# Kernel optimization log

Hardware: AMD Instinct MI355X
Metric: run time of the kernel (lower is better)

The kernel has to match this reference:

```python
import jax, jax.numpy as jnp
import numpy as np

D_MODEL = 1024
NUM_HEADS = 16
D_K = D_MODEL // NUM_HEADS


def setup_inputs() -> dict:
    key = jax.random.key(0)
    ks = jax.random.split(key, 9)
    s = 1.0 / np.sqrt(D_MODEL)
    x = jax.random.normal(ks[0], (4, 2048, D_MODEL), dtype=jnp.float32)
    Wq = jax.random.uniform(ks[1], (D_MODEL, D_MODEL), jnp.float32, -s, s)
    bq = jax.random.uniform(ks[2], (D_MODEL,), jnp.float32, -s, s)
    Wk = jax.random.uniform(ks[3], (D_MODEL, D_MODEL), jnp.float32, -s, s)
    bk = jax.random.uniform(ks[4], (D_MODEL,), jnp.float32, -s, s)
    Wv = jax.random.uniform(ks[5], (D_MODEL, D_MODEL), jnp.float32, -s, s)
    bv = jax.random.uniform(ks[6], (D_MODEL,), jnp.float32, -s, s)
    Wo = jax.random.uniform(ks[7], (D_MODEL, D_MODEL), jnp.float32, -s, s)
    bo = jax.random.uniform(ks[8], (D_MODEL,), jnp.float32, -s, s)
    return {"x": x, "Wq": Wq, "bq": bq, "Wk": Wk, "bk": bk,
            "Wv": Wv, "bv": bv, "Wo": Wo, "bo": bo}


def reference(x, Wq, bq, Wk, bk, Wv, bv, Wo, bo):
    B, S, _ = x.shape
    # Linear projections (torch Linear: x @ W.T + b)
    q = x @ Wq.T + bq
    k = x @ Wk.T + bk
    v = x @ Wv.T + bv
    # [B, H, S, d_k]
    q = q.reshape(B, S, NUM_HEADS, D_K).transpose(0, 2, 1, 3)
    k = k.reshape(B, S, NUM_HEADS, D_K).transpose(0, 2, 1, 3)
    v = v.reshape(B, S, NUM_HEADS, D_K).transpose(0, 2, 1, 3)
    score = jnp.einsum('bhqd,bhkd->bhqk', q, k) / jnp.sqrt(jnp.float32(D_K))
    causal = jnp.tril(jnp.ones((S, S), dtype=bool))  # True = keep
    score = jnp.where(causal[None, None], score, -jnp.inf)
    attn = jax.nn.softmax(score, axis=-1)
    out = jnp.einsum('bhqk,bhkd->bhqd', attn, v)
    out = out.transpose(0, 2, 1, 3).reshape(B, S, D_MODEL)
    return out @ Wo.T + bo
```

## Files before the change

### kernel.cpp

```cpp
#include <hip/hip_runtime.h>
#include <hip/hip_bf16.h>
#include <stdint.h>

#define D_MODEL 1024
#define SEQ     2048
#define BATCH   4
#define NHEAD   16
#define DKH     64
#define MTOT    (BATCH * SEQ)

typedef __bf16 bf16x8 __attribute__((ext_vector_type(8)));
typedef __bf16 bf16x4 __attribute__((ext_vector_type(4)));
typedef float  floatx4 __attribute__((ext_vector_type(4)));
typedef short  s16x4  __attribute__((ext_vector_type(4)));

#define GLOAD_LDS16(gp, lp)                                            \
    __builtin_amdgcn_global_load_lds(                                  \
        (const __attribute__((address_space(1))) unsigned int*)(gp),   \
        (__attribute__((address_space(3))) unsigned int*)(lp), 16, 0, 0)

#define MFMA16(a, b, c) __builtin_amdgcn_mfma_f32_16x16x32_bf16(a, b, c, 0, 0, 0)

#if __has_builtin(__builtin_amdgcn_exp2f)
#define EXP2(x) __builtin_amdgcn_exp2f(x)
#else
#define EXP2(x) exp2f(x)
#endif

static __device__ __forceinline__ floatx4 pv_mfma(s16x4 a, s16x4 b, floatx4 c)
{
#if __has_builtin(__builtin_amdgcn_mfma_f32_16x16x16bf16_1k)
    return __builtin_amdgcn_mfma_f32_16x16x16bf16_1k(a, b, c, 0, 0, 0);
#else
    asm("v_mfma_f32_16x16x16_bf16 %0, %1, %2, %0" : "+v"(c) : "v"(a), "v"(b));
    return c;
#endif
}

__global__ __launch_bounds__(256)
void cvt_x_kernel(const float* __restrict__ src, __bf16* __restrict__ dst)
{
    const int i = (blockIdx.x * 256 + threadIdx.x) * 4;
    floatx4 v = *(const floatx4*)(src + i);
    bf16x4 o;
    o[0] = (__bf16)v[0]; o[1] = (__bf16)v[1]; o[2] = (__bf16)v[2]; o[3] = (__bf16)v[3];
    *(bf16x4*)(dst + i) = o;
}

__global__ __launch_bounds__(256)
void cvt_w3_kernel(const float* __restrict__ Wq, const float* __restrict__ Wk,
                   const float* __restrict__ Wv, __bf16* __restrict__ Wcat)
{
    const int z = blockIdx.y;
    const float* src = (z == 0) ? Wq : ((z == 1) ? Wk : Wv);
    const int i = (blockIdx.x * 256 + threadIdx.x) * 4;
    floatx4 v = *(const floatx4*)(src + i);
    bf16x4 o;
    o[0] = (__bf16)v[0]; o[1] = (__bf16)v[1]; o[2] = (__bf16)v[2]; o[3] = (__bf16)v[3];
    *(bf16x4*)(Wcat + (size_t)z * (D_MODEL * D_MODEL) + i) = o;
}

__global__ __launch_bounds__(256)
void qkv_gemm_kernel(const __bf16* __restrict__ xb, const __bf16* __restrict__ Wcat,
                     const float* __restrict__ bq, const float* __restrict__ bk,
                     const float* __restrict__ bv,
                     __bf16* __restrict__ Q, __bf16* __restrict__ K,
                     __bf16* __restrict__ Vt)
{
    __shared__ __align__(16) char smem_raw[128 * 136 * 2];
    __bf16* As = (__bf16*)smem_raw;
    __bf16* Bs = (__bf16*)(smem_raw + 8192);
    __bf16* Cs = (__bf16*)smem_raw;

    const int t    = threadIdx.x;
    const int w    = t >> 6, l = t & 63, quad = l >> 4, r16 = l & 15;
    const int wm   = w & 1, wn = w >> 1;
    const int m0   = blockIdx.y * 128;
    const int n0   = blockIdx.x * 128;
    const int z    = n0 >> 10;
    const float* bias = (z == 0) ? bq : ((z == 1) ? bk : bv);
    __bf16* outQK     = (z == 0) ? Q  : K;
    const float scale = (z == 0) ? 0.18033688011112042f : 1.0f;

    floatx4 acc[4][4];
#pragma unroll
    for (int i = 0; i < 4; ++i)
#pragma unroll
        for (int j = 0; j < 4; ++j) acc[i][j] = (floatx4){0.f, 0.f, 0.f, 0.f};

    const int c0 = t, c1 = t + 256;
    const int row0 = c0 >> 2, s0 = ((c0 & 3) ^ (row0 & 3)) * 8;
    const int row1 = c1 >> 2, s1 = ((c1 & 3) ^ (row1 & 3)) * 8;
    const __bf16* Ag0 = xb   + (size_t)(m0 + row0) * 1024 + s0;
    const __bf16* Ag1 = xb   + (size_t)(m0 + row1) * 1024 + s1;
    const __bf16* Bg0 = Wcat + (size_t)(n0 + row0) * 1024 + s0;
    const __bf16* Bg1 = Wcat + (size_t)(n0 + row1) * 1024 + s1;
    unsigned int* lAs = (unsigned int*)As;
    unsigned int* lBs = (unsigned int*)Bs;

    const int fsw = (quad ^ (r16 & 3)) * 8;

    for (int k0 = 0; k0 < 1024; k0 += 32) {
        __syncthreads();
        GLOAD_LDS16(Ag0 + k0, lAs + c0 * 4);
        GLOAD_LDS16(Ag1 + k0, lAs + c1 * 4);
        GLOAD_LDS16(Bg0 + k0, lBs + c0 * 4);
        GLOAD_LDS16(Bg1 + k0, lBs + c1 * 4);
        __syncthreads();

        bf16x8 af[4], bfm[4];
#pragma unroll
        for (int i = 0; i < 4; ++i)
            af[i] = *(const bf16x8*)&As[(wm * 64 + i * 16 + r16) * 32 + fsw];
#pragma unroll
        for (int j = 0; j < 4; ++j)
            bfm[j] = *(const bf16x8*)&Bs[(wn * 64 + j * 16 + r16) * 32 + fsw];
#pragma unroll
        for (int i = 0; i < 4; ++i)
#pragma unroll
            for (int j = 0; j < 4; ++j)
                acc[i][j] = MFMA16(af[i], bfm[j], acc[i][j]);
    }

    __syncthreads();

    if (z == 2) {
#pragma unroll
        for (int i = 0; i < 4; ++i) {
            const int mb = wm * 64 + i * 16 + quad * 4;
#pragma unroll
            for (int j = 0; j < 4; ++j) {
                const int nl = wn * 64 + j * 16 + r16;
                const float bb = bias[(n0 + nl) & 1023];
                bf16x4 p4;
#pragma unroll
                for (int r = 0; r < 4; ++r) p4[r] = (__bf16)(acc[i][j][r] + bb);
                *(bf16x4*)&Cs[nl * 136 + mb] = p4;
            }
        }
    } else {
#pragma unroll
        for (int i = 0; i < 4; ++i) {
            const int mb = wm * 64 + i * 16 + quad * 4;
#pragma unroll
            for (int j = 0; j < 4; ++j) {
                const int nl = wn * 64 + j * 16 + r16;
                const float bb = bias[(n0 + nl) & 1023];
#pragma unroll
                for (int r = 0; r < 4; ++r)
                    Cs[(mb + r) * 136 + nl] =
                        (__bf16)((acc[i][j][r] + bb) * scale);
            }
        }
    }
    __syncthreads();

    const int b  = m0 >> 11;
    if (z == 2) {
#pragma unroll
        for (int k = 0; k < 8; ++k) {
            const int nl = (t >> 4) + k * 16;
            const int ml = (t & 15) * 8;
            bf16x8 row = *(const bf16x8*)&Cs[nl * 136 + ml];
            const int f = (n0 + nl) & 1023, h = f >> 6, d = f & 63;
            const int s = (m0 & 2047) + ml;
            *(bf16x8*)&Vt[((size_t)((b * 16 + h) * 64 + d) << 11) + s] = row;
        }
    } else {
#pragma unroll
        for (int k = 0; k < 8; ++k) {
            const int ml = (t >> 4) + k * 16;
            const int nl = (t & 15) * 8;
            bf16x8 row = *(const bf16x8*)&Cs[ml * 136 + nl];
            const int f = (n0 + nl) & 1023, h = f >> 6, d = f & 63;
            const int s = (m0 & 2047) + ml;
            *(bf16x8*)&outQK[((size_t)(b * 16 + h) << 17) + ((size_t)s << 6) + d]
                = row;
        }
    }
}

__global__ __launch_bounds__(256)
void out_gemm_kernel(const __bf16* __restrict__ A, const __bf16* __restrict__ Wob,
                     const float* __restrict__ bo, float* __restrict__ out)
{
    __shared__ __align__(16) __bf16 As[128 * 64];
    __shared__ __align__(16) __bf16 Bs[128 * 64];

    const int t    = threadIdx.x;
    const int w    = t >> 6, l = t & 63, quad = l >> 4, r16 = l & 15;
    const int wm   = w & 1, wn = w >> 1;
    const int m0   = blockIdx.x * 128;
    const int n0   = blockIdx.y * 128;

    floatx4 acc[4][4];
#pragma unroll
    for (int i = 0; i < 4; ++i)
#pragma unroll
        for (int j = 0; j < 4; ++j) acc[i][j] = (floatx4){0.f, 0.f, 0.f, 0.f};

    unsigned int* lAs = (unsigned int*)As;
    unsigned int* lBs = (unsigned int*)Bs;

    const int r0 = t >> 3;
    const __bf16* Agp[4];
    const __bf16* Bgp[4];
#pragma unroll
    for (int i = 0; i < 4; ++i) {
        const int row = r0 + i * 32;
        const int sch8 = ((t & 7) ^ (row & 7)) * 8;
        Agp[i] = A   + (size_t)(m0 + row) * 1024 + sch8;
        Bgp[i] = Wob + (size_t)(n0 + row) * 1024 + sch8;
    }
    const int fsw0 = ((0 * 4 + quad) ^ (r16 & 7)) * 8;
    const int fsw1 = ((1 * 4 + quad) ^ (r16 & 7)) * 8;

    for (int k0 = 0; k0 < 1024; k0 += 64) {
        __syncthreads();
#pragma unroll
        for (int i = 0; i < 4; ++i) {
            const int c = t + 256 * i;
            GLOAD_LDS16(Agp[i] + k0, lAs + c * 4);
            GLOAD_LDS16(Bgp[i] + k0, lBs + c * 4);
        }
        __syncthreads();

#pragma unroll
        for (int kk = 0; kk < 2; ++kk) {
            const int fsw = (kk == 0) ? fsw0 : fsw1;
            bf16x8 af[4], bfm[4];
#pragma unroll
            for (int i = 0; i < 4; ++i)
                af[i] = *(const bf16x8*)&As[(wm * 64 + i * 16 + r16) * 64 + fsw];
#pragma unroll
            for (int j = 0; j < 4; ++j)
                bfm[j] = *(const bf16x8*)&Bs[(wn * 64 + j * 16 + r16) * 64 + fsw];
#pragma unroll
            for (int i = 0; i < 4; ++i)
#pragma unroll
                for (int j = 0; j < 4; ++j)
                    acc[i][j] = MFMA16(af[i], bfm[j], acc[i][j]);
        }
    }

#pragma unroll
    for (int i = 0; i < 4; ++i) {
        const int mg = m0 + wm * 64 + i * 16 + quad * 4;
#pragma unroll
        for (int j = 0; j < 4; ++j) {
            const int ng = n0 + wn * 64 + j * 16 + r16;
            const float bb = bo[ng];
#pragma unroll
            for (int r = 0; r < 4; ++r)
                out[(size_t)(mg + r) * 1024 + ng] = acc[i][j][r] + bb;
        }
    }
}

__global__ __launch_bounds__(256, 4)
void attn_kernel(const __bf16* __restrict__ Qg, const __bf16* __restrict__ Kg,
                 const __bf16* __restrict__ Vtg, __bf16* __restrict__ O)
{
    __shared__ __align__(16) __bf16 Ks[2][64 * 72];
    __shared__ __align__(16) __bf16 Vs[2][64 * 72];

    const int t    = threadIdx.x;
    const int w    = t >> 6, l = t & 63, quad = l >> 4, r16 = l & 15;
    const int bh   = blockIdx.x;
    const int y    = blockIdx.y;
    const int p    = y >> 1, half = y & 1;
    const int qa   = 15 - p, qb = p;
    const size_t base = (size_t)bh * SEQ * DKH;
    const int d0   = 2 * qa + half;
    const int d1   = 2 * qb + half;
    const int nkt  = d0 + 1;
    const int row0 = qa * 128 + half * 64 + w * 16;
    const int row1 = qb * 128 + half * 64 + w * 16;

    const s16x4 ones16 = {(short)0x3F80, (short)0x3F80,
                          (short)0x3F80, (short)0x3F80};

    bf16x8 qf00, qf01, qf10, qf11;
    qf00 = *(const bf16x8*)&Qg[base + (size_t)(row0 + r16) * 64 + quad * 8];
    qf01 = *(const bf16x8*)&Qg[base + (size_t)(row0 + r16) * 64 + 32 + quad * 8];
    qf10 = *(const bf16x8*)&Qg[base + (size_t)(row1 + r16) * 64 + quad * 8];
    qf11 = *(const bf16x8*)&Qg[base + (size_t)(row1 + r16) * 64 + 32 + quad * 8];

    floatx4 o[2][4];
#pragma unroll
    for (int mi = 0; mi < 2; ++mi)
#pragma unroll
        for (int j = 0; j < 4; ++j) o[mi][j] = (floatx4){0.f, 0.f, 0.f, 0.f};
    floatx4 osum[2];
    osum[0] = (floatx4){0.f, 0.f, 0.f, 0.f};
    osum[1] = (floatx4){0.f, 0.f, 0.f, 0.f};

    const int srow = t >> 3;
    const int sg   = (t & 7) * 8;

    bf16x8 kc0, kc1, vc0, vc1;
    kc0 = *(const bf16x8*)&Kg[base + (size_t)srow * 64 + sg];
    kc1 = *(const bf16x8*)&Kg[base + (size_t)(32 + srow) * 64 + sg];
    vc0 = *(const bf16x8*)&Vtg[base + (size_t)srow * 2048 + sg];
    vc1 = *(const bf16x8*)&Vtg[base + (size_t)(32 + srow) * 2048 + sg];

    for (int kt = 0; kt < nkt; ++kt) {
        __bf16* ks = Ks[kt & 1];
        __bf16* vs = Vs[kt & 1];
        *(bf16x8*)&ks[srow * 72 + sg] = kc0;
        *(bf16x8*)&ks[(32 + srow) * 72 + sg] = kc1;
        *(bf16x8*)&vs[srow * 72 + sg] = vc0;
        *(bf16x8*)&vs[(32 + srow) * 72 + sg] = vc1;
        if (kt + 1 < nkt) {
            const int kr = (kt + 1) * 64;
            kc0 = *(const bf16x8*)&Kg[base + (size_t)(kr + srow) * 64 + sg];
            kc1 = *(const bf16x8*)&Kg[base + (size_t)(kr + 32 + srow) * 64 + sg];
            vc0 = *(const bf16x8*)&Vtg[base + (size_t)srow * 2048 + kr + sg];
            vc1 = *(const bf16x8*)&Vtg[base + (size_t)(32 + srow) * 2048 + kr + sg];
        }
        __syncthreads();

        const bool a1 = (kt <= d1);
        __builtin_amdgcn_s_setprio(1);
        bf16x8 kf0, kf1;
#pragma unroll
        for (int j = 0; j < 4; ++j) {
            kf0 = *(const bf16x8*)&ks[(j * 16 + r16) * 72 + quad * 8];
            kf1 = *(const bf16x8*)&ks[(j * 16 + r16) * 72 + 32 + quad * 8];
            floatx4 z0 = (floatx4){0.f, 0.f, 0.f, 0.f};
            floatx4 z1 = (floatx4){0.f, 0.f, 0.f, 0.f};
            z0 = MFMA16(kf0, qf00, z0);
            z0 = MFMA16(kf1, qf01, z0);
            if (a1) {
                z1 = MFMA16(kf0, qf10, z1);
                z1 = MFMA16(kf1, qf11, z1);
            }
            const int kg = kt * 64 + j * 16 + quad * 4;
            bf16x4 pb0, pb1;
            if (kt < d0) {
#pragma unroll
                for (int r = 0; r < 4; ++r)
                    pb0[r] = (__bf16)EXP2(z0[r]);
            } else {
                const int qg0 = row0 + r16;
#pragma unroll
                for (int r = 0; r < 4; ++r) {
                    float pp = 0.f;
                    if (kg + r <= qg0) pp = EXP2(z0[r]);
                    pb0[r] = (__bf16)pp;
                }
            }
            s16x4 pa0 = __builtin_bit_cast(s16x4, pb0);
            s16x4 pa1;
            if (a1) {
                if (kt < d1) {
#pragma unroll
                    for (int r = 0; r < 4; ++r)
                        pb1[r] = (__bf16)EXP2(z1[r]);
                } else {
                    const int qg1 = row1 + r16;
#pragma unroll
                    for (int r = 0; r < 4; ++r) {
                        float pp = 0.f;
                        if (kg + r <= qg1) pp = EXP2(z1[r]);
                        pb1[r] = (__bf16)pp;
                    }
                }
                pa1 = __builtin_bit_cast(s16x4, pb1);
            }
            osum[0] = pv_mfma(pa0, ones16, osum[0]);
            if (a1) osum[1] = pv_mfma(pa1, ones16, osum[1]);
#pragma unroll
            for (int jd = 0; jd < 4; ++jd) {
                const s16x4 vv =
                    *(const s16x4*)&vs[(jd * 16 + r16) * 72 + j * 16 + quad * 4];
                o[0][jd] = pv_mfma(pa0, vv, o[0][jd]);
                if (a1) o[1][jd] = pv_mfma(pa1, vv, o[1][jd]);
            }
        }
        __builtin_amdgcn_s_setprio(0);
    }

    const int b = bh >> 4, h = bh & 15;
#pragma unroll
    for (int mi = 0; mi < 2; ++mi) {
        const int rowb = (mi == 0) ? row0 : row1;
#pragma unroll
        for (int r = 0; r < 4; ++r) {
            const int qrow = rowb + quad * 4 + r;
            const float inv = 1.f / osum[mi][r];
#pragma unroll
            for (int jd = 0; jd < 4; ++jd) {
                const int d = jd * 16 + r16;
                O[((size_t)(b * SEQ + qrow) * D_MODEL) + h * 64 + d] =
                    (__bf16)(o[mi][jd][r] * inv);
            }
        }
    }
}

extern "C" void kernel_launch(void* const* d_in, const int* in_sizes, int n_in,
                              void* d_out, int out_size, void* d_ws, size_t ws_size,
                              hipStream_t stream)
{
    (void)in_sizes; (void)n_in; (void)out_size; (void)ws_size;
    const float* x  = (const float*)d_in[0];
    const float* Wq = (const float*)d_in[1];
    const float* bq = (const float*)d_in[2];
    const float* Wk = (const float*)d_in[3];
    const float* bk = (const float*)d_in[4];
    const float* Wv = (const float*)d_in[5];
    const float* bv = (const float*)d_in[6];
    const float* Wo = (const float*)d_in[7];
    const float* bo = (const float*)d_in[8];
    float* out = (float*)d_out;

    const size_t n_elem = (size_t)MTOT * D_MODEL;
    const int    w_n    = D_MODEL * D_MODEL;
    __bf16* Qb  = (__bf16*)d_out;
    __bf16* xb  = Qb + n_elem;
    __bf16* Kb   = (__bf16*)d_ws;
    __bf16* Vtb  = Kb + n_elem;
    __bf16* Ab   = Vtb + n_elem;
    __bf16* Wcat = Ab;
    __bf16* Wob  = Kb;

    cvt_x_kernel<<<MTOT * D_MODEL / 1024, 256, 0, stream>>>(x, xb);
    cvt_w3_kernel<<<dim3(w_n / 1024, 3), 256, 0, stream>>>(Wq, Wk, Wv, Wcat);
    qkv_gemm_kernel<<<dim3(24, 64), 256, 0, stream>>>(xb, Wcat, bq, bk, bv,
                                                      Qb, Kb, Vtb);
    attn_kernel<<<dim3(64, 16), 256, 0, stream>>>(Qb, Kb, Vtb, Ab);
    cvt_x_kernel<<<w_n / 1024, 256, 0, stream>>>(Wo, Wob);
    out_gemm_kernel<<<dim3(64, 8), 256, 0, stream>>>(Ab, Wob, bo, out);
}
```

Measured before the change: 246.2 us.

## Enlarge QKV GEMM block tile to 256x128 with 512 threads

The QKV projection GEMM now uses 512-thread blocks computing 256x128 output tiles instead of 256x128-thread 128x128 tiles, halving the grid along M. Each B (weight) tile loaded into LDS is reused by twice as many rows, which cuts global weight traffic per FLOP. The epilogue is split into two passes that reuse the same LDS staging buffer, adding extra barriers. Fewer blocks (768) and higher LDS per block may reduce occupancy and latency hiding.

```diff
diff --git a/kernel.cpp b/kernel.cpp
--- a/kernel.cpp
+++ b/kernel.cpp
@@ -60,22 +60,22 @@
     *(bf16x4*)(Wcat + (size_t)z * (D_MODEL * D_MODEL) + i) = o;
 }
 
-__global__ __launch_bounds__(256)
+__global__ __launch_bounds__(512)
 void qkv_gemm_kernel(const __bf16* __restrict__ xb, const __bf16* __restrict__ Wcat,
                      const float* __restrict__ bq, const float* __restrict__ bk,
                      const float* __restrict__ bv,
                      __bf16* __restrict__ Q, __bf16* __restrict__ K,
                      __bf16* __restrict__ Vt)
 {
-    __shared__ __align__(16) char smem_raw[128 * 136 * 2];
+    __shared__ __align__(16) char smem_raw[34816];
     __bf16* As = (__bf16*)smem_raw;
-    __bf16* Bs = (__bf16*)(smem_raw + 8192);
+    __bf16* Bs = (__bf16*)(smem_raw + 16384);
     __bf16* Cs = (__bf16*)smem_raw;
 
     const int t    = threadIdx.x;
     const int w    = t >> 6, l = t & 63, quad = l >> 4, r16 = l & 15;
-    const int wm   = w & 1, wn = w >> 1;
-    const int m0   = blockIdx.y * 128;
+    const int wm   = w >> 1, wn = w & 1;
+    const int m0   = blockIdx.y * 256;
     const int n0   = blockIdx.x * 128;
     const int z    = n0 >> 10;
     const float* bias = (z == 0) ? bq : ((z == 1) ? bk : bv);
@@ -88,13 +88,13 @@
 #pragma unroll
         for (int j = 0; j < 4; ++j) acc[i][j] = (floatx4){0.f, 0.f, 0.f, 0.f};
 
-    const int c0 = t, c1 = t + 256;
-    const int row0 = c0 >> 2, s0 = ((c0 & 3) ^ (row0 & 3)) * 8;
-    const int row1 = c1 >> 2, s1 = ((c1 & 3) ^ (row1 & 3)) * 8;
-    const __bf16* Ag0 = xb   + (size_t)(m0 + row0) * 1024 + s0;
-    const __bf16* Ag1 = xb   + (size_t)(m0 + row1) * 1024 + s1;
-    const __bf16* Bg0 = Wcat + (size_t)(n0 + row0) * 1024 + s0;
-    const __bf16* Bg1 = Wcat + (size_t)(n0 + row1) * 1024 + s1;
+    const int cA0 = t, cA1 = t + 512, cB = t;
+    const int rA0 = cA0 >> 2, sA0 = ((cA0 & 3) ^ (rA0 & 3)) * 8;
+    const int rA1 = cA1 >> 2, sA1 = ((cA1 & 3) ^ (rA1 & 3)) * 8;
+    const int rB  = cB >> 2,  sB  = ((cB & 3) ^ (rB & 3)) * 8;
+    const __bf16* Ag0 = xb   + (size_t)(m0 + rA0) * 1024 + sA0;
+    const __bf16* Ag1 = xb   + (size_t)(m0 + rA1) * 1024 + sA1;
+    const __bf16* Bg  = Wcat + (size_t)(n0 + rB) * 1024 + sB;
     unsigned int* lAs = (unsigned int*)As;
     unsigned int* lBs = (unsigned int*)Bs;
 
@@ -102,10 +102,9 @@
 
     for (int k0 = 0; k0 < 1024; k0 += 32) {
         __syncthreads();
-        GLOAD_LDS16(Ag0 + k0, lAs + c0 * 4);
-        GLOAD_LDS16(Ag1 + k0, lAs + c1 * 4);
-        GLOAD_LDS16(Bg0 + k0, lBs + c0 * 4);
-        GLOAD_LDS16(Bg1 + k0, lBs + c1 * 4);
+        GLOAD_LDS16(Ag0 + k0, lAs + cA0 * 4);
+        GLOAD_LDS16(Ag1 + k0, lAs + cA1 * 4);
+        GLOAD_LDS16(Bg  + k0, lBs + cB * 4);
         __syncthreads();
 
         bf16x8 af[4], bfm[4];
@@ -122,60 +121,68 @@
                 acc[i][j] = MFMA16(af[i], bfm[j], acc[i][j]);
     }
 
-    __syncthreads();
-
-    if (z == 2) {
-#pragma unroll
-        for (int i = 0; i < 4; ++i) {
-            const int mb = wm * 64 + i * 16 + quad * 4;
-#pragma unroll
-            for (int j = 0; j < 4; ++j) {
-                const int nl = wn * 64 + j * 16 + r16;
-                const float bb = bias[(n0 + nl) & 1023];
-                bf16x4 p4;
-#pragma unroll
-                for (int r = 0; r < 4; ++r) p4[r] = (__bf16)(acc[i][j][r] + bb);
-                *(bf16x4*)&Cs[nl * 136 + mb] = p4;
-            }
-        }
-    } else {
-#pragma unroll
-        for (int i = 0; i < 4; ++i) {
-            const int mb = wm * 64 + i * 16 + quad * 4;
-#pragma unroll
-            for (int j = 0; j < 4; ++j) {
-                const int nl = wn * 64 + j * 16 + r16;
-                const float bb = bias[(n0 + nl) & 1023];
-#pragma unroll
-                for (int r = 0; r < 4; ++r)
-                    Cs[(mb + r) * 136 + nl] =
-                        (__bf16)((acc[i][j][r] + bb) * scale);
-            }
-        }
-    }
-    __syncthreads();
-
-    const int b  = m0 >> 11;
-    if (z == 2) {
-#pragma unroll
-        for (int k = 0; k < 8; ++k) {
-            const int nl = (t >> 4) + k * 16;
-            const int ml = (t & 15) * 8;
-            bf16x8 row = *(const bf16x8*)&Cs[nl * 136 + ml];
-            const int f = (n0 + nl) & 1023, h = f >> 6, d = f & 63;
-            const int s = (m0 & 2047) + ml;
-            *(bf16x8*)&Vt[((size_t)((b * 16 + h) * 64 + d) << 11) + s] = row;
-        }
-    } else {
-#pragma unroll
-        for (int k = 0; k < 8; ++k) {
-            const int ml = (t >> 4) + k * 16;
-            const int nl = (t & 15) * 8;
-            bf16x8 row = *(const bf16x8*)&Cs[ml * 136 + nl];
-            const int f = (n0 + nl) & 1023, h = f >> 6, d = f & 63;
-            const int s = (m0 & 2047) + ml;
-            *(bf16x8*)&outQK[((size_t)(b * 16 + h) << 17) + ((size_t)s << 6) + d]
-                = row;
+    const int b = m0 >> 11;
+#pragma unroll
+    for (int pass = 0; pass < 2; ++pass) {
+        __syncthreads();
+        const bool active = ((wm >> 1) == pass);
+        const int  mhw    = wm & 1;
+        if (z == 2) {
+            if (active) {
+#pragma unroll
+                for (int i = 0; i < 4; ++i) {
+                    const int mbl = mhw * 64 + i * 16 + quad * 4;
+#pragma unroll
+                    for (int j = 0; j < 4; ++j) {
+                        const int nl = wn * 64 + j * 16 + r16;
+                        const float bb = bias[(n0 + nl) & 1023];
+                        bf16x4 p4;
+#pragma unroll
+                        for (int r = 0; r < 4; ++r)
+                            p4[r] = (__bf16)(acc[i][j][r] + bb);
+                        *(bf16x4*)&Cs[nl * 136 + mbl] = p4;
+                    }
+                }
+            }
+            __syncthreads();
+#pragma unroll
+            for (int k = 0; k < 4; ++k) {
+                const int id  = t + 512 * k;
+                const int nll = id >> 4;
+                const int ml  = (id & 15) * 8;
+                bf16x8 rowv = *(const bf16x8*)&Cs[nll * 136 + ml];
+                const int f = (n0 + nll) & 1023, h = f >> 6, d = f & 63;
+                const int s = (m0 & 2047) + pass * 128 + ml;
+                *(bf16x8*)&Vt[((size_t)((b * 16 + h) * 64 + d) << 11) + s] = rowv;
+            }
+        } else {
+            if (active) {
+#pragma unroll
+                for (int i = 0; i < 4; ++i) {
+                    const int mbl = mhw * 64 + i * 16 + quad * 4;
+#pragma unroll
+                    for (int j = 0; j < 4; ++j) {
+                        const int nl = wn * 64 + j * 16 + r16;
+                        const float bb = bias[(n0 + nl) & 1023];
+#pragma unroll
+                        for (int r = 0; r < 4; ++r)
+                            Cs[(mbl + r) * 136 + nl] =
+                                (__bf16)((acc[i][j][r] + bb) * scale);
+                    }
+                }
+            }
+            __syncthreads();
+#pragma unroll
+            for (int k = 0; k < 4; ++k) {
+                const int id  = t + 512 * k;
+                const int mll = id >> 4;
+                const int nl  = (id & 15) * 8;
+                bf16x8 rowv = *(const bf16x8*)&Cs[mll * 136 + nl];
+                const int f = (n0 + nl) & 1023, h = f >> 6, d = f & 63;
+                const int s = (m0 & 2047) + pass * 128 + mll;
+                *(bf16x8*)&outQK[((size_t)(b * 16 + h) << 17) + ((size_t)s << 6) + d]
+                    = rowv;
+            }
         }
     }
 }
@@ -427,7 +434,7 @@
 
     cvt_x_kernel<<<MTOT * D_MODEL / 1024, 256, 0, stream>>>(x, xb);
     cvt_w3_kernel<<<dim3(w_n / 1024, 3), 256, 0, stream>>>(Wq, Wk, Wv, Wcat);
-    qkv_gemm_kernel<<<dim3(24, 64), 256, 0, stream>>>(xb, Wcat, bq, bk, bv,
+    qkv_gemm_kernel<<<dim3(24, 32), 512, 0, stream>>>(xb, Wcat, bq, bk, bv,
                                                       Qb, Kb, Vtb);
     attn_kernel<<<dim3(64, 16), 256, 0, stream>>>(Qb, Kb, Vtb, Ab);
     cvt_x_kernel<<<w_n / 1024, 256, 0, stream>>>(Wo, Wob);
```

Result: slower. 254.6 us (+3.4%).
